# Optimization experiments

Measured on AMD Instinct MI355X. Metric: run time of the kernel, lower is better.

The kernel has to match this reference:

```python
import jax, jax.numpy as jnp
import numpy as np

N = 100000
E = 3200000
D_IN = 128
D_H = 128
K = 3


def setup_inputs() -> dict:
    key = jax.random.key(0)
    ks = jax.random.split(key, 8)
    x = jax.random.normal(ks[0], (N, D_IN), dtype=jnp.float32)
    src = jax.random.randint(ks[1], (E,), 0, N, dtype=jnp.int32)
    dst = jax.random.randint(ks[2], (E,), 0, N, dtype=jnp.int32)
    s = 1.0 / np.sqrt(D_H)
    W1 = jax.random.normal(ks[3], (D_IN, D_H), dtype=jnp.float32) * s
    b1 = jnp.zeros((D_H,), jnp.float32)
    W2 = jax.random.normal(ks[4], (D_H, D_H), dtype=jnp.float32) * s
    b2 = jnp.zeros((D_H,), jnp.float32)
    Wf1 = jax.random.normal(ks[5], (D_H, D_H), dtype=jnp.float32) * s
    bf1 = jnp.zeros((D_H,), jnp.float32)
    Wf2 = jax.random.normal(ks[6], (D_H, 1), dtype=jnp.float32) * s
    bf2 = jnp.zeros((1,), jnp.float32)
    return {"x": x, "src": src, "dst": dst, "W1": W1, "b1": b1, "W2": W2,
            "b2": b2, "Wf1": Wf1, "bf1": bf1, "Wf2": Wf2, "bf2": bf2}


def _sg_propagate(h, src, dst, norm, k):
    # DGL SGConv: k hops of h <- D^{-1/2} A D^{-1/2} h (in-degree norm, clamp>=1)
    for _ in range(k):
        h = h * norm                                   # [N, d]
        h = jax.ops.segment_sum(h[src], dst, num_segments=N)  # SpMM hop
        h = h * norm
    return h


def reference(x, src, dst, W1, b1, W2, b2, Wf1, bf1, Wf2, bf2):
    deg = jax.ops.segment_sum(jnp.ones((E,), jnp.float32), dst, num_segments=N)
    norm = jnp.clip(deg, 1.0, None) ** -0.5            # [N]
    norm = norm[:, None]
    # conv_1: SGConv(k=3) -> linear -> ReLU
    h = _sg_propagate(x, src, dst, norm, K)
    h = jax.nn.relu(h @ W1 + b1)
    # conv_2
    h = _sg_propagate(h, src, dst, norm, K)
    h = jax.nn.relu(h @ W2 + b2)
    # dgl.mean_nodes over the single graph -> [1, D_H]
    hg = jnp.mean(h, axis=0, keepdims=True)
    h = jax.nn.relu(hg @ Wf1 + bf1)
    out = jax.nn.relu(h @ Wf2 + bf2)
    return jax.nn.sigmoid(out)                         # [1, 1]
```

## Files before the change

kernel.cpp:

```cpp
#include <hip/hip_runtime.h>
#include <hip/hip_fp16.h>
#include <math.h>

#define NN 100000
#define EE 3200000
#define D 128
#define NB 391
#define NBLK2 1024
#define ECH2 (EE / NBLK2)
#define NSTRIP (NN / 32)

#define SCALE_R 6.0f
#define SCALE_G 512.0f
#define WSCALE  16.0f
#define PRE1 (1.0f / (216.0f * WSCALE))
#define PRE2 (1.0f / (216.0f * SCALE_G * WSCALE))

typedef float floatx16 __attribute__((ext_vector_type(16)));
typedef float v2f __attribute__((ext_vector_type(2)));

__global__ __launch_bounds__(256) void block_hist(const int* __restrict__ dst,
                                                  int* __restrict__ bh) {
    __shared__ int hist[NB];
    for (int i = threadIdx.x; i < NB; i += 256) hist[i] = 0;
    __syncthreads();
    int e0 = blockIdx.x * ECH2;
    for (int e = e0 + threadIdx.x; e < e0 + ECH2; e += 256)
        atomicAdd(&hist[dst[e] >> 8], 1);
    __syncthreads();
    for (int i = threadIdx.x; i < NB; i += 256)
        bh[i * NBLK2 + blockIdx.x] = hist[i];
}

__global__ __launch_bounds__(256) void bin_scan(int* __restrict__ bh,
                                                int* __restrict__ bintot) {
    __shared__ int ts[256];
    int i = blockIdx.x;
    int t = threadIdx.x;
    int4 v = ((int4*)(bh + i * NBLK2))[t];
    int s = v.x + v.y + v.z + v.w;
    ts[t] = s;
    __syncthreads();
    for (int off = 1; off < 256; off <<= 1) {
        int x = (t >= off) ? ts[t - off] : 0;
        __syncthreads();
        ts[t] += x;
        __syncthreads();
    }
    int run = ts[t] - s;
    int4 o;
    o.x = run; o.y = run + v.x; o.z = o.y + v.y; o.w = o.z + v.z;
    ((int4*)(bh + i * NBLK2))[t] = o;
    if (t == 255) bintot[i] = ts[255];
}

__global__ __launch_bounds__(512) void tiny_scan(const int* __restrict__ bintot,
                                                 int* __restrict__ coff) {
    __shared__ int s[512];
    int t = threadIdx.x;
    int v = (t < NB) ? bintot[t] : 0;
    s[t] = v;
    __syncthreads();
    for (int off = 1; off < 512; off <<= 1) {
        int x = (t >= off) ? s[t - off] : 0;
        __syncthreads();
        s[t] += x;
        __syncthreads();
    }
    int excl = s[t] - v;
    if (t <= NB) coff[t] = excl;
}

__global__ __launch_bounds__(256) void scatter2(const int* __restrict__ src,
                                                const int* __restrict__ dst,
                                                const int* __restrict__ bh,
                                                const int* __restrict__ coff,
                                                int2* __restrict__ ebuf) {
    __shared__ int base[NB];
    int b = blockIdx.x;
    for (int i = threadIdx.x; i < NB; i += 256)
        base[i] = coff[i] + bh[i * NBLK2 + b];
    __syncthreads();
    int e0 = b * ECH2;
    for (int e = e0 + threadIdx.x; e < e0 + ECH2; e += 256) {
        int d = dst[e];
        int pos = atomicAdd(&base[d >> 8], 1);
        ebuf[pos] = make_int2(src[e], d);
    }
}

__global__ __launch_bounds__(256) void fine_sort(const long long* __restrict__ ebuf,
                                                 const int* __restrict__ coarse_off,
                                                 int* __restrict__ rowptr,
                                                 float* __restrict__ norm,
                                                 int* __restrict__ csr) {
    __shared__ int cnt[256];
    __shared__ int sbuf[256];
    int b = blockIdx.x;
    int t = threadIdx.x;
    int e0 = coarse_off[b], e1 = coarse_off[b + 1];
    int n0 = b << 8;
    cnt[t] = 0;
    __syncthreads();
    for (int e = e0 + t; e < e1; e += 256) {
        long long pv = ebuf[e];
        atomicAdd(&cnt[(int)(pv >> 32) & 255], 1);
    }
    __syncthreads();
    int myc = cnt[t];
    sbuf[t] = myc;
    __syncthreads();
    for (int off = 1; off < 256; off <<= 1) {
        int x = (t >= off) ? sbuf[t - off] : 0;
        __syncthreads();
        sbuf[t] += x;
        __syncthreads();
    }
    int excl = sbuf[t] - myc;
    int node = n0 + t;
    if (node < NN) {
        rowptr[node] = e0 + excl;
        float dd = (float)myc;
        if (dd < 1.0f) dd = 1.0f;
        norm[node] = rsqrtf(dd);
    }
    cnt[t] = e0 + excl;
    __syncthreads();
    for (int e = e0 + t; e < e1; e += 256) {
        long long pv = __builtin_nontemporal_load(ebuf + e);
        int pos = atomicAdd(&cnt[(int)(pv >> 32) & 255], 1);
        csr[pos] = (int)pv << 7;
    }
    if (b == 0 && t == 0) rowptr[NN] = EE;
}

__global__ void conv_w_fp8(const float* __restrict__ W, char* __restrict__ Wt8) {
    int idx = blockIdx.x * 256 + threadIdx.x;
    if (idx < D * D / 2) {
        int n = idx >> 6, k2 = (idx & 63) * 2;
        float a = W[k2 * D + n] * WSCALE;
        float b = W[(k2 + 1) * D + n] * WSCALE;
        int pk = __builtin_amdgcn_cvt_pk_fp8_f32(a, b, 0, 0);
        ((short*)Wt8)[idx] = (short)(pk & 0xffff);
    }
}

__global__ void convert_scale_fp8(const float4* __restrict__ x4, int* __restrict__ g,
                                  const float* __restrict__ norm) {
    int idx = blockIdx.x * 256 + threadIdx.x;
    if (idx < NN * 32) {
        int row = idx >> 5;
        float n = norm[row];
        float4 v = x4[idx];
        int w = __builtin_amdgcn_cvt_pk_fp8_f32(v.x * n, v.y * n, 0, 0);
        w = __builtin_amdgcn_cvt_pk_fp8_f32(v.z * n, v.w * n, w, 1);
        g[idx] = w;
    }
}

template <int FINAL>
__global__ __launch_bounds__(256) void gather_fp8(const int* __restrict__ rowptr,
                                                  const int* __restrict__ csr,
                                                  const char* __restrict__ hs,
                                                  const float* __restrict__ norm,
                                                  char* __restrict__ outv, float post) {
    int node = blockIdx.x * 4 + (threadIdx.x >> 6);
    int lane = threadIdx.x & 63;
    int e = lane >> 4;
    int c = lane & 15;
    int p0 = rowptr[node], p1 = rowptr[node + 1];
    float nrm = norm[node];
    v2f acc[4];
#pragma unroll
    for (int i = 0; i < 4; ++i) acc[i] = (v2f)(0.0f);
    int coff8 = c << 3;
    int p = p0 + e;
#define CVT_ACC(v) { \
        acc[0] += __builtin_amdgcn_cvt_pk_f32_fp8((v).x, 0); \
        acc[1] += __builtin_amdgcn_cvt_pk_f32_fp8((v).x, 1); \
        acc[2] += __builtin_amdgcn_cvt_pk_f32_fp8((v).y, 0); \
        acc[3] += __builtin_amdgcn_cvt_pk_f32_fp8((v).y, 1); }
    int s0 = 0, s1 = 0, s2 = 0, s3 = 0;
    if (p + 12 < p1) { s0 = csr[p]; s1 = csr[p + 4]; s2 = csr[p + 8]; s3 = csr[p + 12]; }
    while (p + 12 < p1) {
        int2 v0 = *(const int2*)(hs + (unsigned)s0 + coff8);
        int2 v1 = *(const int2*)(hs + (unsigned)s1 + coff8);
        int2 v2 = *(const int2*)(hs + (unsigned)s2 + coff8);
        int2 v3 = *(const int2*)(hs + (unsigned)s3 + coff8);
        p += 16;
        if (p + 12 < p1) {
            s0 = csr[p]; s1 = csr[p + 4]; s2 = csr[p + 8]; s3 = csr[p + 12];
        }
        CVT_ACC(v0);
        CVT_ACC(v1);
        CVT_ACC(v2);
        CVT_ACC(v3);
    }
    for (; p + 4 < p1; p += 8) {
        int t0 = csr[p];
        int t1 = csr[p + 4];
        int2 v0 = *(const int2*)(hs + (unsigned)t0 + coff8);
        int2 v1 = *(const int2*)(hs + (unsigned)t1 + coff8);
        CVT_ACC(v0);
        CVT_ACC(v1);
    }
    if (p < p1) {
        int t0 = csr[p];
        int2 v0 = *(const int2*)(hs + (unsigned)t0 + coff8);
        CVT_ACC(v0);
    }
#undef CVT_ACC
#pragma unroll
    for (int off = 16; off < 64; off <<= 1) {
#pragma unroll
        for (int i = 0; i < 4; ++i) {
            acc[i].x += __shfl_xor(acc[i].x, off, 64);
            acc[i].y += __shfl_xor(acc[i].y, off, 64);
        }
    }
    if (e == 0) {
        float m = (FINAL ? nrm : nrm * nrm) * post;
        int2 w;
        w.x = __builtin_amdgcn_cvt_pk_fp8_f32(acc[0].x * m, acc[0].y * m, 0, 0);
        w.x = __builtin_amdgcn_cvt_pk_fp8_f32(acc[1].x * m, acc[1].y * m, w.x, 1);
        w.y = __builtin_amdgcn_cvt_pk_fp8_f32(acc[2].x * m, acc[2].y * m, 0, 0);
        w.y = __builtin_amdgcn_cvt_pk_fp8_f32(acc[3].x * m, acc[3].y * m, w.y, 1);
        *(int2*)(outv + (unsigned)node * 128 + coff8) = w;
    }
}

__global__ __launch_bounds__(256) void gemm1_mfma(const char* __restrict__ H8,
                                                  const char* __restrict__ Wt8,
                                                  const float* __restrict__ b,
                                                  const float* __restrict__ norm,
                                                  char* __restrict__ out8) {
    int lane = threadIdx.x & 63;
    int w = threadIdx.x >> 6;
    int m = lane & 31;
    int q = lane >> 5;
    int col = w * 32 + m;
    long bf[8];
    const long* wp = (const long*)(Wt8 + (size_t)col * D + q * 8);
#pragma unroll
    for (int kc = 0; kc < 8; ++kc) bf[kc] = wp[kc * 2];
    float bc = b[col];
    for (int s = blockIdx.x; s < NSTRIP; s += gridDim.x) {
        int r0 = s * 32;
        floatx16 acc;
#pragma unroll
        for (int i = 0; i < 16; ++i) acc[i] = 0.0f;
        const long* ap = (const long*)(H8 + (size_t)(r0 + m) * D + q * 8);
#pragma unroll
        for (int kc = 0; kc < 8; ++kc)
            acc = __builtin_amdgcn_mfma_f32_32x32x16_fp8_fp8(ap[kc * 2], bf[kc], acc, 0, 0, 0);
#pragma unroll
        for (int r = 0; r < 16; ++r) {
            int row = r0 + (r & 3) + 8 * (r >> 2) + 4 * q;
            float v = fmaxf(acc[r] * PRE1 + bc, 0.0f) * norm[row] * SCALE_G;
            int pk = __builtin_amdgcn_cvt_pk_fp8_f32(v, v, 0, 0);
            out8[(size_t)row * D + col] = (char)(pk & 0xff);
        }
    }
}

__global__ __launch_bounds__(256) void gemm2_mfma_colsum(const char* __restrict__ H8,
                                                         const char* __restrict__ Wt8,
                                                         const float* __restrict__ b,
                                                         float* __restrict__ colsum) {
    int lane = threadIdx.x & 63;
    int w = threadIdx.x >> 6;
    int m = lane & 31;
    int q = lane >> 5;
    int col = w * 32 + m;
    long bf[8];
    const long* wp = (const long*)(Wt8 + (size_t)col * D + q * 8);
#pragma unroll
    for (int kc = 0; kc < 8; ++kc) bf[kc] = wp[kc * 2];
    float bc = b[col];
    float csum = 0.0f;
    for (int s = blockIdx.x; s < NSTRIP; s += gridDim.x) {
        int r0 = s * 32;
        floatx16 acc;
#pragma unroll
        for (int i = 0; i < 16; ++i) acc[i] = 0.0f;
        const long* ap = (const long*)(H8 + (size_t)(r0 + m) * D + q * 8);
#pragma unroll
        for (int kc = 0; kc < 8; ++kc)
            acc = __builtin_amdgcn_mfma_f32_32x32x16_fp8_fp8(ap[kc * 2], bf[kc], acc, 0, 0, 0);
#pragma unroll
        for (int r = 0; r < 16; ++r) csum += fmaxf(acc[r] * PRE2 + bc, 0.0f);
    }
    csum += __shfl_down(csum, 32);
    if (lane < 32) atomicAdd(&colsum[col], csum);
}

__global__ __launch_bounds__(128) void final_mlp(const float* __restrict__ colsum,
                                                 const float* __restrict__ Wf1,
                                                 const float* __restrict__ bf1,
                                                 const float* __restrict__ Wf2,
                                                 const float* __restrict__ bf2,
                                                 float* __restrict__ out) {
    __shared__ float hg[D];
    __shared__ float red[D];
    int j = threadIdx.x;
    hg[j] = colsum[j] * (1.0f / (float)NN);
    __syncthreads();
    float acc = bf1[j];
#pragma unroll 16
    for (int k = 0; k < D; ++k)
        acc = fmaf(hg[k], Wf1[k * D + j], acc);
    acc = fmaxf(acc, 0.0f);
    red[j] = acc * Wf2[j];
    __syncthreads();
    for (int s = 64; s > 0; s >>= 1) {
        if (j < s) red[j] += red[j + s];
        __syncthreads();
    }
    if (j == 0) {
        float o = red[0] + bf2[0];
        o = fmaxf(o, 0.0f);
        out[0] = 1.0f / (1.0f + expf(-o));
    }
}

extern "C" void kernel_launch(void* const* d_in, const int* in_sizes, int n_in,
                              void* d_out, int out_size, void* d_ws, size_t ws_size,
                              hipStream_t stream) {
    const float* x   = (const float*)d_in[0];
    const int*   src = (const int*)d_in[1];
    const int*   dst = (const int*)d_in[2];
    const float* W1  = (const float*)d_in[3];
    const float* b1  = (const float*)d_in[4];
    const float* W2  = (const float*)d_in[5];
    const float* b2  = (const float*)d_in[6];
    const float* Wf1 = (const float*)d_in[7];
    const float* bf1 = (const float*)d_in[8];
    const float* Wf2 = (const float*)d_in[9];
    const float* bf2 = (const float*)d_in[10];
    float* out = (float*)d_out;

    char* ws = (char*)d_ws;
    constexpr size_t OFF_BT   = 0;
    constexpr size_t OFF_CO   = 2048;
    constexpr size_t OFF_CS   = 4096;
    constexpr size_t OFF_WT1  = 8192;
    constexpr size_t OFF_WT2  = OFF_WT1 + 16384;
    constexpr size_t OFF_RP   = OFF_WT2 + 16384;
    constexpr size_t OFF_NORM = OFF_RP + 400128;
    constexpr size_t OFF_BH   = OFF_NORM + 400128;
    constexpr size_t OFF_EBUF = OFF_BH + (size_t)NB * NBLK2 * 4;
    constexpr size_t OFF_CSR  = OFF_EBUF + (size_t)EE * 8;
    constexpr size_t OFF_A8   = OFF_CSR + (size_t)EE * 4;
    constexpr size_t OFF_B8   = OFF_A8 + (size_t)NN * D;
    int*    bintot = (int*)(ws + OFF_BT);
    int*    coff   = (int*)(ws + OFF_CO);
    float*  colsum = (float*)(ws + OFF_CS);
    char*   Wt1    = ws + OFF_WT1;
    char*   Wt2    = ws + OFF_WT2;
    int*    rowptr = (int*)(ws + OFF_RP);
    float*  norm   = (float*)(ws + OFF_NORM);
    int*    bh     = (int*)(ws + OFF_BH);
    int2*   ebuf   = (int2*)(ws + OFF_EBUF);
    int*    csr    = (int*)(ws + OFF_CSR);
    char*   bufA8  = ws + OFF_A8;
    char*   bufB8  = ws + OFF_B8;

    const int nT = 256;
    const int gridC = (NN * 32 + nT - 1) / nT;
    const int gridG = NN / 4;

    block_hist<<<NBLK2, 256, 0, stream>>>(dst, bh);
    bin_scan<<<NB, 256, 0, stream>>>(bh, bintot);
    tiny_scan<<<1, 512, 0, stream>>>(bintot, coff);
    scatter2<<<NBLK2, 256, 0, stream>>>(src, dst, bh, coff, ebuf);
    fine_sort<<<NB, 256, 0, stream>>>((const long long*)ebuf, coff, rowptr, norm, csr);

    conv_w_fp8<<<32, 256, 0, stream>>>(W1, Wt1);
    conv_w_fp8<<<32, 256, 0, stream>>>(W2, Wt2);

    convert_scale_fp8<<<gridC, nT, 0, stream>>>((const float4*)x, (int*)bufA8, norm);
    gather_fp8<0><<<gridG, 256, 0, stream>>>(rowptr, csr, bufA8, norm, bufB8, SCALE_R);
    gather_fp8<0><<<gridG, 256, 0, stream>>>(rowptr, csr, bufB8, norm, bufA8, SCALE_R);
    gather_fp8<1><<<gridG, 256, 0, stream>>>(rowptr, csr, bufA8, norm, bufB8, SCALE_R);

    gemm1_mfma<<<625, 256, 0, stream>>>(bufB8, Wt1, b1, norm, bufA8);

    gather_fp8<0><<<gridG, 256, 0, stream>>>(rowptr, csr, bufA8, norm, bufB8, SCALE_R);
    gather_fp8<0><<<gridG, 256, 0, stream>>>(rowptr, csr, bufB8, norm, bufA8, SCALE_R);
    gather_fp8<1><<<gridG, 256, 0, stream>>>(rowptr, csr, bufA8, norm, bufB8, SCALE_R);

    hipMemsetAsync(colsum, 0, D * 4, stream);
    gemm2_mfma_colsum<<<250, 256, 0, stream>>>(bufB8, Wt2, b2, colsum);

    final_mlp<<<1, 128, 0, stream>>>(colsum, Wf1, bf1, Wf2, bf2, out);
}
```

Before: 588.1 us.

## Stage fine-sort edges in LDS, merge weight conversions, fuse final MLP into gemm2

fine_sort now copies up to 7168 edges of its bucket into shared memory on the first pass. The second pass reads them from LDS instead of reloading them from global memory, with a fallback for overflow. The two weight-conversion launches are merged into one, and the final MLP runs in the last-finishing block of gemm2 using a done counter. This drops two kernel launches, but the 56KB LDS array may reduce fine_sort occupancy.

```diff
diff --git a/kernel.cpp b/kernel.cpp
--- a/kernel.cpp
+++ b/kernel.cpp
@@ -9,6 +9,8 @@
 #define NBLK2 1024
 #define ECH2 (EE / NBLK2)
 #define NSTRIP (NN / 32)
+#define FS_CAP 7168
+#define GRID_G2 250
 
 #define SCALE_R 6.0f
 #define SCALE_G 512.0f
@@ -96,14 +98,22 @@
                                                  int* __restrict__ csr) {
     __shared__ int cnt[256];
     __shared__ int sbuf[256];
+    __shared__ long long es[FS_CAP];
     int b = blockIdx.x;
     int t = threadIdx.x;
     int e0 = coarse_off[b], e1 = coarse_off[b + 1];
+    int n = e1 - e0;
+    int nl = n < FS_CAP ? n : FS_CAP;
     int n0 = b << 8;
     cnt[t] = 0;
     __syncthreads();
-    for (int e = e0 + t; e < e1; e += 256) {
-        long long pv = ebuf[e];
+    for (int i = t; i < nl; i += 256) {
+        long long pv = ebuf[e0 + i];
+        es[i] = pv;
+        atomicAdd(&cnt[(int)(pv >> 32) & 255], 1);
+    }
+    for (int i = FS_CAP + t; i < n; i += 256) {
+        long long pv = ebuf[e0 + i];
         atomicAdd(&cnt[(int)(pv >> 32) & 255], 1);
     }
     __syncthreads();
@@ -126,16 +136,25 @@
     }
     cnt[t] = e0 + excl;
     __syncthreads();
-    for (int e = e0 + t; e < e1; e += 256) {
-        long long pv = __builtin_nontemporal_load(ebuf + e);
+    for (int i = t; i < nl; i += 256) {
+        long long pv = es[i];
         int pos = atomicAdd(&cnt[(int)(pv >> 32) & 255], 1);
         csr[pos] = (int)pv << 7;
     }
+    for (int i = FS_CAP + t; i < n; i += 256) {
+        long long pv = __builtin_nontemporal_load(ebuf + e0 + i);
+        int pos = atomicAdd(&cnt[(int)(pv >> 32) & 255], 1);
+        csr[pos] = (int)pv << 7;
+    }
     if (b == 0 && t == 0) rowptr[NN] = EE;
 }
 
-__global__ void conv_w_fp8(const float* __restrict__ W, char* __restrict__ Wt8) {
-    int idx = blockIdx.x * 256 + threadIdx.x;
+__global__ void conv_w2_fp8(const float* __restrict__ W1, const float* __restrict__ W2,
+                            char* __restrict__ Wt1, char* __restrict__ Wt2) {
+    int g = blockIdx.x;
+    const float* W = (g < 32) ? W1 : W2;
+    char* Wt8 = (g < 32) ? Wt1 : Wt2;
+    int idx = (g & 31) * 256 + threadIdx.x;
     if (idx < D * D / 2) {
         int n = idx >> 6, k2 = (idx & 63) * 2;
         float a = W[k2 * D + n] * WSCALE;
@@ -266,7 +285,13 @@
 __global__ __launch_bounds__(256) void gemm2_mfma_colsum(const char* __restrict__ H8,
                                                          const char* __restrict__ Wt8,
                                                          const float* __restrict__ b,
-                                                         float* __restrict__ colsum) {
+                                                         float* __restrict__ colsum,
+                                                         int* __restrict__ done,
+                                                         const float* __restrict__ Wf1,
+                                                         const float* __restrict__ bf1,
+                                                         const float* __restrict__ Wf2,
+                                                         const float* __restrict__ bf2,
+                                                         float* __restrict__ out) {
     int lane = threadIdx.x & 63;
     int w = threadIdx.x >> 6;
     int m = lane & 31;
@@ -292,25 +317,27 @@
     }
     csum += __shfl_down(csum, 32);
     if (lane < 32) atomicAdd(&colsum[col], csum);
-}
-
-__global__ __launch_bounds__(128) void final_mlp(const float* __restrict__ colsum,
-                                                 const float* __restrict__ Wf1,
-                                                 const float* __restrict__ bf1,
-                                                 const float* __restrict__ Wf2,
-                                                 const float* __restrict__ bf2,
-                                                 float* __restrict__ out) {
+
+    __threadfence();
+    __shared__ int isLast;
+    if (threadIdx.x == 0)
+        isLast = (atomicAdd(done, 1) == GRID_G2 - 1);
+    __syncthreads();
+    if (!isLast) return;
+
     __shared__ float hg[D];
     __shared__ float red[D];
     int j = threadIdx.x;
-    hg[j] = colsum[j] * (1.0f / (float)NN);
-    __syncthreads();
-    float acc = bf1[j];
+    if (j < D) hg[j] = atomicAdd(&colsum[j], 0.0f) * (1.0f / (float)NN);
+    __syncthreads();
+    if (j < D) {
+        float acc2 = bf1[j];
 #pragma unroll 16
-    for (int k = 0; k < D; ++k)
-        acc = fmaf(hg[k], Wf1[k * D + j], acc);
-    acc = fmaxf(acc, 0.0f);
-    red[j] = acc * Wf2[j];
+        for (int k = 0; k < D; ++k)
+            acc2 = fmaf(hg[k], Wf1[k * D + j], acc2);
+        acc2 = fmaxf(acc2, 0.0f);
+        red[j] = acc2 * Wf2[j];
+    }
     __syncthreads();
     for (int s = 64; s > 0; s >>= 1) {
         if (j < s) red[j] += red[j + s];
@@ -355,6 +382,7 @@
     int*    bintot = (int*)(ws + OFF_BT);
     int*    coff   = (int*)(ws + OFF_CO);
     float*  colsum = (float*)(ws + OFF_CS);
+    int*    done   = (int*)(ws + OFF_CS + 512);
     char*   Wt1    = ws + OFF_WT1;
     char*   Wt2    = ws + OFF_WT2;
     int*    rowptr = (int*)(ws + OFF_RP);
@@ -375,8 +403,7 @@
     scatter2<<<NBLK2, 256, 0, stream>>>(src, dst, bh, coff, ebuf);
     fine_sort<<<NB, 256, 0, stream>>>((const long long*)ebuf, coff, rowptr, norm, csr);
 
-    conv_w_fp8<<<32, 256, 0, stream>>>(W1, Wt1);
-    conv_w_fp8<<<32, 256, 0, stream>>>(W2, Wt2);
+    conv_w2_fp8<<<64, 256, 0, stream>>>(W1, W2, Wt1, Wt2);
 
     convert_scale_fp8<<<gridC, nT, 0, stream>>>((const float4*)x, (int*)bufA8, norm);
     gather_fp8<0><<<gridG, 256, 0, stream>>>(rowptr, csr, bufA8, norm, bufB8, SCALE_R);
@@ -389,8 +416,7 @@
     gather_fp8<0><<<gridG, 256, 0, stream>>>(rowptr, csr, bufB8, norm, bufA8, SCALE_R);
     gather_fp8<1><<<gridG, 256, 0, stream>>>(rowptr, csr, bufA8, norm, bufB8, SCALE_R);
 
-    hipMemsetAsync(colsum, 0, D * 4, stream);
-    gemm2_mfma_colsum<<<250, 256, 0, stream>>>(bufB8, Wt2, b2, colsum);
-
-    final_mlp<<<1, 128, 0, stream>>>(colsum, Wf1, bf1, Wf2, bf2, out);
-}
+    hipMemsetAsync(colsum, 0, 768, stream);
+    gemm2_mfma_colsum<<<GRID_G2, 256, 0, stream>>>(bufB8, Wt2, b2, colsum, done,
+                                                   Wf1, bf1, Wf2, bf2, out);
+}
```

Result: no change. 585.7 us (-0.4%).
